# Kernel tuning notes

Measured on AMD Instinct MI355X. Metric: run time of the kernel, lower is better.

Reference implementation:

```python
import jax, jax.numpy as jnp
import numpy as np

# Dims: B=batch, T=seq, D=input=256=F*F, H=hidden=256=F*F, F=16 factor, R=16 TT rank, 4 gates (I,F,G,O)
F, R, NG = 16, 16, 4


def setup_inputs():
    key = jax.random.key(0)
    ks = jax.random.split(key, 11)
    s = 0.1  # core init scale keeps gate pre-activations O(1)
    inp = {
        "x": jax.random.normal(ks[0], (64, 1024, 256), jnp.float32),
        # TT cores for the 4 input-to-hidden gates (boundary ranks squeezed)
        "ih_g0": s * jax.random.normal(ks[1], (NG, F, R), jnp.float32),
        "ih_g1": s * jax.random.normal(ks[2], (NG, R, F, R), jnp.float32),
        "ih_g2": s * jax.random.normal(ks[3], (NG, R, F, R), jnp.float32),
        "ih_g3": s * jax.random.normal(ks[4], (NG, R, F), jnp.float32),
        "ih_bias": jnp.zeros((NG, F * F), jnp.float32),
        # TT cores for the 4 hidden-to-hidden gates
        "hh_g0": s * jax.random.normal(ks[5], (NG, F, R), jnp.float32),
        "hh_g1": s * jax.random.normal(ks[6], (NG, R, F, R), jnp.float32),
        "hh_g2": s * jax.random.normal(ks[7], (NG, R, F, R), jnp.float32),
        "hh_g3": s * jax.random.normal(ks[8], (NG, R, F), jnp.float32),
        "hh_bias": jnp.zeros((NG, F * F), jnp.float32),
    }
    return inp


def tt_linear(x2, g0, g1, g2, g3, bias):
    # x2: [N, F*F] -> contract TT cores per gate g -> [N, NG, F*F]
    n = x2.shape[0]
    x3 = x2.reshape(n, F, F)
    t = jnp.einsum('bmn,gmr->bgnr', x3, g0)      # contract first input factor
    t = jnp.einsum('bgnr,grns->bgs', t, g1)      # contract second input factor
    t = jnp.einsum('bgs,gsot->bgot', t, g2)      # emit first output factor
    y = jnp.einsum('bgot,gtp->bgop', t, g3)      # emit second output factor
    return y.reshape(n, NG, F * F) + bias        # bias: [NG, F*F]


def reference(x, ih_g0, ih_g1, ih_g2, ih_g3, ih_bias,
              hh_g0, hh_g1, hh_g2, hh_g3, hh_bias):
    B, T, D = x.shape
    H = F * F
    # Precompute input-to-hidden gate contributions for all timesteps at once
    ih_all = tt_linear(x.reshape(B * T, D), ih_g0, ih_g1, ih_g2, ih_g3, ih_bias)
    ih_all = ih_all.reshape(B, T, NG, H).transpose(1, 0, 2, 3)  # [T,B,4,H]

    def step(carry, ih_t):
        h, c = carry
        gates = ih_t + tt_linear(h, hh_g0, hh_g1, hh_g2, hh_g3, hh_bias)
        i = jax.nn.sigmoid(gates[:, 0])
        f = jax.nn.sigmoid(gates[:, 1])
        g = jnp.tanh(gates[:, 2])
        o = jax.nn.sigmoid(gates[:, 3])
        c = f * c + i * g
        h = o * jnp.tanh(c)
        return (h, c), h

    h0 = jnp.zeros((B, H), x.dtype)
    c0 = jnp.zeros((B, H), x.dtype)
    (h, c), ys = jax.lax.scan(step, (h0, c0), ih_all)
    output = ys.transpose(1, 0, 2)  # [B,T,H]
    return output, (h, c)
```

## Files before the change

### kernel.cpp

```cpp
#include <hip/hip_runtime.h>


#define WS_A1I 0
#define WS_A1H 16384
#define WS_C2I 32768
#define WS_C2H 49152
#define WS_BIAS 65536
#define WS_T2 66560

__device__ __forceinline__ float fsig(float x) {
    float e = __builtin_amdgcn_exp2f(-1.442695040888963f * x);
    return __builtin_amdgcn_rcpf(1.0f + e);
}
__device__ __forceinline__ float ftanh_(float x) {
    float e = __builtin_amdgcn_exp2f(2.885390081777926f * x);
    return 1.0f - 2.0f * __builtin_amdgcn_rcpf(1.0f + e);
}

__device__ __forceinline__ void bar_lds() {
    asm volatile("s_waitcnt lgkmcnt(0)\n\ts_barrier" ::: "memory");
}

__global__ void k_compose(const float* __restrict__ g0i, const float* __restrict__ g1i,
                          const float* __restrict__ g2i, const float* __restrict__ g3i,
                          const float* __restrict__ bi,
                          const float* __restrict__ g0h, const float* __restrict__ g1h,
                          const float* __restrict__ g2h, const float* __restrict__ g3h,
                          const float* __restrict__ bh,
                          float* __restrict__ ws) {
    int id = blockIdx.x * 256 + threadIdx.x;
    if (id < 16384) {
        int g = id >> 12, s = (id >> 8) & 15, mn = id & 255;
        int m = mn >> 4, n = mn & 15;
        float aI = 0.f, aH = 0.f;
        for (int r = 0; r < 16; ++r) {
            aI += g0i[(g * 16 + m) * 16 + r] * g1i[((g * 16 + r) * 16 + n) * 16 + s];
            aH += g0h[(g * 16 + m) * 16 + r] * g1h[((g * 16 + r) * 16 + n) * 16 + s];
        }
        ws[WS_A1I + (g * 16 + s) * 256 + mn] = aI;
        ws[WS_A1H + (g * 16 + s) * 256 + mn] = aH;
    } else if (id < 32768) {
        int id2 = id - 16384;
        int g = id2 >> 12, s = (id2 >> 8) & 15, j = id2 & 255;
        int o = j >> 4, p = j & 15;
        float aI = 0.f, aH = 0.f;
        for (int t = 0; t < 16; ++t) {
            aI += g2i[((g * 16 + s) * 16 + o) * 16 + t] * g3i[(g * 16 + t) * 16 + p];
            aH += g2h[((g * 16 + s) * 16 + o) * 16 + t] * g3h[(g * 16 + t) * 16 + p];
        }
        ws[WS_C2I + (g * 16 + s) * 256 + j] = aI;
        ws[WS_C2H + (g * 16 + s) * 256 + j] = aH;
    } else if (id < 33792) {
        int id2 = id - 32768;
        ws[WS_BIAS + id2] = bi[id2] + bh[id2];
    }
}

__global__ __launch_bounds__(256, 2) void k_t2ih(const float* __restrict__ x,
                                                 const float* __restrict__ ws,
                                                 float* __restrict__ T2) {
    __shared__ __align__(16) float Xs[64 * 256];
    __shared__ __align__(16) float As[64 * 256];
    const int tid = threadIdx.x;
    const long r0 = (long)blockIdx.x * 64;

    const float4* X4 = (const float4*)(x + r0 * 256);
    const float4* A4 = (const float4*)(ws + WS_A1I);
    float4* Xs4 = (float4*)Xs;
    float4* As4 = (float4*)As;
#pragma unroll
    for (int k = 0; k < 16; ++k) {
        int idx = tid + k * 256;
        int row = idx >> 6, c = idx & 63;
        int sw = (row << 6) | (c ^ (row & 15));
        Xs4[sw] = X4[idx];
        As4[sw] = A4[idx];
    }
    __syncthreads();

    const int ro = tid & 15;
    const int q  = tid >> 4;
    float acc[4][4];
#pragma unroll
    for (int i = 0; i < 4; ++i)
#pragma unroll
        for (int j = 0; j < 4; ++j) acc[i][j] = 0.f;

    for (int mn4 = 0; mn4 < 64; ++mn4) {
        float4 a[4], xv[4];
#pragma unroll
        for (int j = 0; j < 4; ++j) {
            int row = ro * 4 + j;
            a[j] = As4[(row << 6) | (mn4 ^ (row & 15))];
        }
#pragma unroll
        for (int i = 0; i < 4; ++i) {
            int row = q * 4 + i;
            xv[i] = Xs4[(row << 6) | (mn4 ^ (row & 15))];
        }
#pragma unroll
        for (int i = 0; i < 4; ++i)
#pragma unroll
            for (int j = 0; j < 4; ++j)
                acc[i][j] += xv[i].x * a[j].x + xv[i].y * a[j].y +
                             xv[i].z * a[j].z + xv[i].w * a[j].w;
    }
#pragma unroll
    for (int i = 0; i < 4; ++i)
#pragma unroll
        for (int j = 0; j < 4; ++j)
            T2[(r0 + q * 4 + i) * 64 + ro * 4 + j] = acc[i][j];
}

__global__ __launch_bounds__(512, 2) void k_lstm(const float* __restrict__ ws,
                                                 const float* __restrict__ T2,
                                                 float* __restrict__ out) {
    __shared__ __align__(16) float hS[256];
    __shared__ __align__(16) float t2hS[64];
    __shared__ __align__(16) float t2iS[2][64];
    __shared__ __align__(16) float gS[4 * 256];

    const int tid  = threadIdx.x;
    const int w    = tid >> 6;
    const int lane = tid & 63;
    const int b    = blockIdx.x;

    const int ch   = lane >> 3;
    const int u_ab = 8 * w + (lane & 7);
    float a1r[32];
    {
        const float4* A1h4 = (const float4*)(ws + WS_A1H);
#pragma unroll
        for (int k = 0; k < 8; ++k) {
            float4 v = A1h4[u_ab * 64 + ch * 8 + k];
            a1r[4 * k + 0] = v.x; a1r[4 * k + 1] = v.y;
            a1r[4 * k + 2] = v.z; a1r[4 * k + 3] = v.w;
        }
    }

    const int g  = w >> 1;
    const int j0 = (w & 1) * 64 + lane;
    const int j1 = j0 + 128;
    float c2h0[16], c2h1[16], c2i0[16], c2i1[16];
#pragma unroll
    for (int s = 0; s < 16; ++s) {
        c2h0[s] = ws[WS_C2H + (16 * g + s) * 256 + j0];
        c2h1[s] = ws[WS_C2H + (16 * g + s) * 256 + j1];
        c2i0[s] = ws[WS_C2I + (16 * g + s) * 256 + j0];
        c2i1[s] = ws[WS_C2I + (16 * g + s) * 256 + j1];
    }
    float bias0 = ws[WS_BIAS + g * 256 + j0];
    float bias1 = ws[WS_BIAS + g * 256 + j1];

#pragma unroll
    for (int i = 0; i < 32; ++i) asm volatile("" : "+v"(a1r[i]));
#pragma unroll
    for (int i = 0; i < 16; ++i)
        asm volatile("" : "+v"(c2h0[i]), "+v"(c2h1[i]), "+v"(c2i0[i]), "+v"(c2i1[i]));

    float c = 0.f, h_last = 0.f;
    if (tid < 256) hS[tid] = 0.f;
    const float* T2b = T2 + (long)b * 1024 * 64;
    float4 preA = make_float4(0.f, 0.f, 0.f, 0.f);
    float4 preB = make_float4(0.f, 0.f, 0.f, 0.f);
    if (tid < 16) {
        ((float4*)t2iS[0])[tid] = ((const float4*)T2b)[tid];
        preA = ((const float4*)(T2b + 64))[tid];
    }
    bar_lds();

    float* outB = out + (long)b * 1024 * 256;
    const float4* hS4  = (const float4*)hS;
    const float4* t2hv = (const float4*)t2hS;

    auto body = [&](int t, float4& preW, float4& preL) {
        float p0 = 0.f, p1 = 0.f, p2 = 0.f, p3 = 0.f;
#pragma unroll
        for (int k = 0; k < 8; ++k) {
            float4 hv = hS4[ch * 8 + ((k + ch) & 7)];
            p0 += hv.x * a1r[4 * k + 0];
            p1 += hv.y * a1r[4 * k + 1];
            p2 += hv.z * a1r[4 * k + 2];
            p3 += hv.w * a1r[4 * k + 3];
        }
        float t2v = (p0 + p1) + (p2 + p3);
        if ((tid < 16) && (t + 2 < 1024))
            preL = ((const float4*)(T2b + (t + 2) * 64))[tid];
        t2v += __shfl_xor(t2v, 8);
        t2v += __shfl_xor(t2v, 16);
        t2v += __shfl_xor(t2v, 32);
        if (lane < 8) t2hS[8 * w + lane] = t2v;

        bar_lds();

        if ((tid < 16) && (t + 1 < 1024))
            ((float4*)t2iS[(t + 1) & 1])[tid] = preW;

        const float4* t2iv = (const float4*)t2iS[t & 1];
        float acc0 = bias0, acc1 = bias1;
#pragma unroll
        for (int q = 0; q < 4; ++q) {
            float4 th = t2hv[g * 4 + q];
            float4 ti = t2iv[g * 4 + q];
            acc0 += th.x * c2h0[4*q+0] + th.y * c2h0[4*q+1] + th.z * c2h0[4*q+2] + th.w * c2h0[4*q+3]
                  + ti.x * c2i0[4*q+0] + ti.y * c2i0[4*q+1] + ti.z * c2i0[4*q+2] + ti.w * c2i0[4*q+3];
            acc1 += th.x * c2h1[4*q+0] + th.y * c2h1[4*q+1] + th.z * c2h1[4*q+2] + th.w * c2h1[4*q+3]
                  + ti.x * c2i1[4*q+0] + ti.y * c2i1[4*q+1] + ti.z * c2i1[4*q+2] + ti.w * c2i1[4*q+3];
        }
        gS[g * 256 + j0] = acc0;
        gS[g * 256 + j1] = acc1;

        bar_lds();

        if (tid < 256) {
            float gi = gS[tid], gf = gS[256 + tid], gg = gS[512 + tid], go = gS[768 + tid];
            float ig = fsig(gi), fg = fsig(gf), gv = ftanh_(gg), og = fsig(go);
            c = fg * c + ig * gv;
            float h = og * ftanh_(c);
            h_last = h;
            outB[t * 256 + tid] = h;
            int chj = tid >> 5, kj = (tid >> 2) & 7;
            hS[chj * 32 + (((kj + chj) & 7) << 2) + (tid & 3)] = h;
        }

        bar_lds();
    };

    for (int t = 0; t < 1024; t += 2) {
        body(t, preA, preB);
        body(t + 1, preB, preA);
    }

    if (tid < 256) {
        out[16777216 + b * 256 + tid] = h_last;
        out[16777216 + 16384 + b * 256 + tid] = c;
    }
}

extern "C" void kernel_launch(void* const* d_in, const int* in_sizes, int n_in,
                              void* d_out, int out_size, void* d_ws, size_t ws_size,
                              hipStream_t stream) {
    const float* x     = (const float*)d_in[0];
    const float* ih_g0 = (const float*)d_in[1];
    const float* ih_g1 = (const float*)d_in[2];
    const float* ih_g2 = (const float*)d_in[3];
    const float* ih_g3 = (const float*)d_in[4];
    const float* ih_b  = (const float*)d_in[5];
    const float* hh_g0 = (const float*)d_in[6];
    const float* hh_g1 = (const float*)d_in[7];
    const float* hh_g2 = (const float*)d_in[8];
    const float* hh_g3 = (const float*)d_in[9];
    const float* hh_b  = (const float*)d_in[10];
    float* out = (float*)d_out;
    float* ws  = (float*)d_ws;

    k_compose<<<132, 256, 0, stream>>>(ih_g0, ih_g1, ih_g2, ih_g3, ih_b,
                                       hh_g0, hh_g1, hh_g2, hh_g3, hh_b, ws);
    k_t2ih<<<1024, 256, 0, stream>>>(x, ws, ws + WS_T2);
    k_lstm<<<64, 512, 0, stream>>>(ws, ws + WS_T2, out);
}
```

Before: 1.025 ms.

## Double LSTM block to 1024 threads, reduce hidden projection via LDS atomics

The recurrent kernel now launches 1024 threads per batch row, so each thread computes one gate output instead of two and holds half as many weights in registers. The first-stage h projection is split across 16 lanes per rank unit, and the partial sums are combined with shared-memory atomicAdd instead of a shuffle tree. The gate buffer is transposed so each cell thread reads all four gates as a single float4. The aim is to shorten the per-timestep serial critical path, at the cost of barriers across 16 waves, LDS atomic contention, and an extra reset of t2hS every step.

New measurement: 2.688 ms. +162.3%, slower.

```diff
diff --git a/kernel.cpp b/kernel.cpp
--- a/kernel.cpp
+++ b/kernel.cpp
@@ -112,115 +112,109 @@
             T2[(r0 + q * 4 + i) * 64 + ro * 4 + j] = acc[i][j];
 }
 
-__global__ __launch_bounds__(512, 2) void k_lstm(const float* __restrict__ ws,
-                                                 const float* __restrict__ T2,
-                                                 float* __restrict__ out) {
+__global__ __launch_bounds__(1024, 4) void k_lstm(const float* __restrict__ ws,
+                                                  const float* __restrict__ T2,
+                                                  float* __restrict__ out) {
     __shared__ __align__(16) float hS[256];
     __shared__ __align__(16) float t2hS[64];
     __shared__ __align__(16) float t2iS[2][64];
-    __shared__ __align__(16) float gS[4 * 256];
+    __shared__ __align__(16) float gS[256 * 4];
 
     const int tid  = threadIdx.x;
     const int w    = tid >> 6;
     const int lane = tid & 63;
     const int b    = blockIdx.x;
 
-    const int ch   = lane >> 3;
-    const int u_ab = 8 * w + (lane & 7);
-    float a1r[32];
+    const int u   = 4 * w + (lane >> 4);
+    const int sub = lane & 15;
+    float a1r[16];
     {
         const float4* A1h4 = (const float4*)(ws + WS_A1H);
 #pragma unroll
-        for (int k = 0; k < 8; ++k) {
-            float4 v = A1h4[u_ab * 64 + ch * 8 + k];
-            a1r[4 * k + 0] = v.x; a1r[4 * k + 1] = v.y;
-            a1r[4 * k + 2] = v.z; a1r[4 * k + 3] = v.w;
-        }
-    }
-
-    const int g  = w >> 1;
-    const int j0 = (w & 1) * 64 + lane;
-    const int j1 = j0 + 128;
-    float c2h0[16], c2h1[16], c2i0[16], c2i1[16];
+        for (int kk = 0; kk < 4; ++kk) {
+            float4 v = A1h4[u * 64 + sub * 4 + kk];
+            a1r[4 * kk + 0] = v.x; a1r[4 * kk + 1] = v.y;
+            a1r[4 * kk + 2] = v.z; a1r[4 * kk + 3] = v.w;
+        }
+    }
+
+    const int g = w >> 2;
+    const int j = (w & 3) * 64 + lane;
+    float c2h[16], c2i[16];
 #pragma unroll
     for (int s = 0; s < 16; ++s) {
-        c2h0[s] = ws[WS_C2H + (16 * g + s) * 256 + j0];
-        c2h1[s] = ws[WS_C2H + (16 * g + s) * 256 + j1];
-        c2i0[s] = ws[WS_C2I + (16 * g + s) * 256 + j0];
-        c2i1[s] = ws[WS_C2I + (16 * g + s) * 256 + j1];
-    }
-    float bias0 = ws[WS_BIAS + g * 256 + j0];
-    float bias1 = ws[WS_BIAS + g * 256 + j1];
-
-#pragma unroll
-    for (int i = 0; i < 32; ++i) asm volatile("" : "+v"(a1r[i]));
+        c2h[s] = ws[WS_C2H + (16 * g + s) * 256 + j];
+        c2i[s] = ws[WS_C2I + (16 * g + s) * 256 + j];
+    }
+    float bias = ws[WS_BIAS + g * 256 + j];
+
 #pragma unroll
     for (int i = 0; i < 16; ++i)
-        asm volatile("" : "+v"(c2h0[i]), "+v"(c2h1[i]), "+v"(c2i0[i]), "+v"(c2i1[i]));
+        asm volatile("" : "+v"(a1r[i]), "+v"(c2h[i]), "+v"(c2i[i]));
+    asm volatile("" : "+v"(bias));
+
+    const int hIdx = 64 * ((tid >> 2) & 3) + 4 * (tid >> 4) + (tid & 3);
 
     float c = 0.f, h_last = 0.f;
     if (tid < 256) hS[tid] = 0.f;
+    if (tid < 64) t2hS[tid] = 0.f;
     const float* T2b = T2 + (long)b * 1024 * 64;
+    const float4* T2b4 = (const float4*)T2b;
     float4 preA = make_float4(0.f, 0.f, 0.f, 0.f);
     float4 preB = make_float4(0.f, 0.f, 0.f, 0.f);
     if (tid < 16) {
-        ((float4*)t2iS[0])[tid] = ((const float4*)T2b)[tid];
-        preA = ((const float4*)(T2b + 64))[tid];
+        ((float4*)t2iS[0])[tid] = T2b4[tid];
+        preA = T2b4[16 + tid];
     }
     bar_lds();
 
     float* outB = out + (long)b * 1024 * 256;
     const float4* hS4  = (const float4*)hS;
-    const float4* t2hv = (const float4*)t2hS;
+    const float4* th4  = (const float4*)t2hS;
 
     auto body = [&](int t, float4& preW, float4& preL) {
-        float p0 = 0.f, p1 = 0.f, p2 = 0.f, p3 = 0.f;
-#pragma unroll
-        for (int k = 0; k < 8; ++k) {
-            float4 hv = hS4[ch * 8 + ((k + ch) & 7)];
-            p0 += hv.x * a1r[4 * k + 0];
-            p1 += hv.y * a1r[4 * k + 1];
-            p2 += hv.z * a1r[4 * k + 2];
-            p3 += hv.w * a1r[4 * k + 3];
-        }
-        float t2v = (p0 + p1) + (p2 + p3);
+        float4 s4 = make_float4(0.f, 0.f, 0.f, 0.f);
+#pragma unroll
+        for (int kk = 0; kk < 4; ++kk) {
+            float4 hv = hS4[kk * 16 + sub];
+            s4.x += hv.x * a1r[4 * kk + 0];
+            s4.y += hv.y * a1r[4 * kk + 1];
+            s4.z += hv.z * a1r[4 * kk + 2];
+            s4.w += hv.w * a1r[4 * kk + 3];
+        }
+        atomicAdd(&t2hS[u], (s4.x + s4.y) + (s4.z + s4.w));
+
         if ((tid < 16) && (t + 2 < 1024))
-            preL = ((const float4*)(T2b + (t + 2) * 64))[tid];
-        t2v += __shfl_xor(t2v, 8);
-        t2v += __shfl_xor(t2v, 16);
-        t2v += __shfl_xor(t2v, 32);
-        if (lane < 8) t2hS[8 * w + lane] = t2v;
+            preL = T2b4[(t + 2) * 16 + tid];
 
         bar_lds();
 
         if ((tid < 16) && (t + 1 < 1024))
             ((float4*)t2iS[(t + 1) & 1])[tid] = preW;
 
-        const float4* t2iv = (const float4*)t2iS[t & 1];
-        float acc0 = bias0, acc1 = bias1;
+        const float4* ti4 = (const float4*)t2iS[t & 1];
+        float acc = bias;
 #pragma unroll
         for (int q = 0; q < 4; ++q) {
-            float4 th = t2hv[g * 4 + q];
-            float4 ti = t2iv[g * 4 + q];
-            acc0 += th.x * c2h0[4*q+0] + th.y * c2h0[4*q+1] + th.z * c2h0[4*q+2] + th.w * c2h0[4*q+3]
-                  + ti.x * c2i0[4*q+0] + ti.y * c2i0[4*q+1] + ti.z * c2i0[4*q+2] + ti.w * c2i0[4*q+3];
-            acc1 += th.x * c2h1[4*q+0] + th.y * c2h1[4*q+1] + th.z * c2h1[4*q+2] + th.w * c2h1[4*q+3]
-                  + ti.x * c2i1[4*q+0] + ti.y * c2i1[4*q+1] + ti.z * c2i1[4*q+2] + ti.w * c2i1[4*q+3];
-        }
-        gS[g * 256 + j0] = acc0;
-        gS[g * 256 + j1] = acc1;
+            float4 th = th4[g * 4 + q];
+            float4 ti = ti4[g * 4 + q];
+            acc += th.x * c2h[4*q+0] + th.y * c2h[4*q+1] + th.z * c2h[4*q+2] + th.w * c2h[4*q+3]
+                 + ti.x * c2i[4*q+0] + ti.y * c2i[4*q+1] + ti.z * c2i[4*q+2] + ti.w * c2i[4*q+3];
+        }
+        gS[j * 4 + g] = acc;
 
         bar_lds();
 
         if (tid < 256) {
-            float gi = gS[tid], gf = gS[256 + tid], gg = gS[512 + tid], go = gS[768 + tid];
-            float ig = fsig(gi), fg = fsig(gf), gv = ftanh_(gg), og = fsig(go);
-            c = fg * c + ig * gv;
+            float4 gv = ((const float4*)gS)[tid];
+            float ig = fsig(gv.x), fg = fsig(gv.y), gg = ftanh_(gv.z), og = fsig(gv.w);
+            c = fg * c + ig * gg;
             float h = og * ftanh_(c);
             h_last = h;
             outB[t * 256 + tid] = h;
-            int chj = tid >> 5, kj = (tid >> 2) & 7;
-            hS[chj * 32 + (((kj + chj) & 7) << 2) + (tid & 3)] = h;
+            hS[hIdx] = h;
+        } else if (tid < 320) {
+            t2hS[tid - 256] = 0.f;
         }
 
         bar_lds();
@@ -257,5 +251,5 @@
     k_compose<<<132, 256, 0, stream>>>(ih_g0, ih_g1, ih_g2, ih_g3, ih_b,
                                        hh_g0, hh_g1, hh_g2, hh_g3, hh_b, ws);
     k_t2ih<<<1024, 256, 0, stream>>>(x, ws, ws + WS_T2);
-    k_lstm<<<64, 512, 0, stream>>>(ws, ws + WS_T2, out);
-}
+    k_lstm<<<64, 1024, 0, stream>>>(ws, ws + WS_T2, out);
+}
```
